# Kernel optimization log

Measured on AMD Instinct MI355X. Metric: run time of the kernel, lower is better.

The kernel has to match this reference:

```python
import jax, jax.numpy as jnp
import numpy as np
from jax import lax

SHIFT_SIZE = 5
PAD = SHIFT_SIZE // 2


def _shift(xn, axis):
    """xn: (B, C, Hp, Wp, Dp) zero-padded volume. Split channels into
    SHIFT_SIZE chunks and roll each chunk by shift in [-PAD, PAD] along `axis`."""
    chunks = jnp.split(xn, SHIFT_SIZE, axis=1)
    shifted = [jnp.roll(c, s, axis=axis) for c, s in zip(chunks, range(-PAD, PAD + 1))]
    return jnp.concatenate(shifted, axis=1)


def _shift_tokens(x, H, W, D, axis):
    """x: (B, N, C) tokens -> shifted tokens (B, N, C). axis=2 shifts H, axis=3 shifts W."""
    B, N, C = x.shape
    xn = x.transpose(0, 2, 1).reshape(B, C, H, W, D)
    xn = jnp.pad(xn, ((0, 0), (0, 0), (PAD, PAD), (PAD, PAD), (PAD, PAD)))
    xs = _shift(xn, axis)
    xs = xs[:, :, PAD:PAD + H, PAD:PAD + W, PAD:PAD + D]
    return xs.reshape(B, C, N).transpose(0, 2, 1)


def setup_inputs() -> dict:
    key = jax.random.key(0)
    ks = jax.random.split(key, 4)
    B, H, W, D = 2, 32, 32, 32
    N = H * W * D
    Cin, Ch = 160, 640
    return {
        "x": jax.random.normal(ks[0], (B, N, Cin), jnp.float32),
        "fc1_w": jax.random.normal(ks[1], (Ch, Cin), jnp.float32) * 0.02,
        "fc1_b": jnp.zeros((Ch,), jnp.float32),
        "dw_w": jax.random.normal(ks[2], (Ch, 1, 3, 3, 3), jnp.float32) * (2.0 / 27.0) ** 0.5,
        "dw_b": jnp.zeros((Ch,), jnp.float32),
        "fc2_w": jax.random.normal(ks[3], (Cin, Ch), jnp.float32) * 0.02,
        "fc2_b": jnp.zeros((Cin,), jnp.float32),
        "H": H, "W": W, "D": D,
    }


def reference(x, fc1_w, fc1_b, dw_w, dw_b, fc2_w, fc2_b, H, W, D):
    B, N, Cin = x.shape
    Ch = fc1_w.shape[0]
    # shift block 1: roll along H (axis 2)
    xs = _shift_tokens(x, H, W, D, axis=2)
    # fc1
    h = jnp.einsum('bnc,hc->bnh', xs, fc1_w) + fc1_b  # (B, N, Ch)
    # depthwise 3x3x3 conv
    hv = h.transpose(0, 2, 1).reshape(B, Ch, H, W, D)
    hv = lax.conv_general_dilated(
        hv, dw_w, window_strides=(1, 1, 1), padding='SAME',
        feature_group_count=Ch,
        dimension_numbers=('NCDHW', 'OIDHW', 'NCDHW'))
    hv = hv + dw_b[None, :, None, None, None]
    hv = jax.nn.gelu(hv, approximate=False)
    h = hv.reshape(B, Ch, N).transpose(0, 2, 1)
    # shift block 2: roll along W (axis 3)
    hs = _shift_tokens(h, H, W, D, axis=3)
    # fc2
    out = jnp.einsum('bnh,oh->bno', hs, fc2_w) + fc2_b  # (B, N, Cin)
    return out
```

## Files before the change

### kernel.cpp

```cpp
#include <hip/hip_runtime.h>
#include <hip/hip_bf16.h>
#include <math.h>

#define DEVI __device__ __forceinline__

typedef __bf16 bf16;
typedef _Float16 f16;
typedef bf16 bf16x4 __attribute__((ext_vector_type(4)));
typedef bf16 bf16x8 __attribute__((ext_vector_type(8)));
typedef f16 f16x8 __attribute__((ext_vector_type(8)));
typedef float f32x4 __attribute__((ext_vector_type(4)));

constexpr int Bb = 2, Hh = 32, Ww = 32, Dd = 32;
constexpr int Nn = Hh * Ww * Dd;
constexpr int BN = Bb * Nn;
constexpr int CIN = 160, CHH = 640;
constexpr int PD = 34;
constexpr int PT = PD * PD * PD;

constexpr size_t W1_OFF  = 0;
constexpr size_t W2_OFF  = W1_OFF + (size_t)CHH * CIN * 2;
constexpr size_t WTH_OFF = W2_OFF + (size_t)CIN * CHH * 2;
constexpr size_t ZP_OFF  = WTH_OFF + 34816;
constexpr size_t U_OFF   = 458752;
constexpr size_t H1P_OFF = U_OFF + (size_t)BN * CHH * 2;

DEVI void async16(const void* g, void* l) {
  __builtin_amdgcn_global_load_lds(
      (const __attribute__((address_space(1))) void*)g,
      (__attribute__((address_space(3))) void*)l, 16, 0, 0);
}

__global__ __launch_bounds__(256) void k_prep_x(const float* __restrict__ x,
                                                bf16* __restrict__ xb, int n4) {
  int i = blockIdx.x * 256 + threadIdx.x;
  if (i >= n4) return;
  float4 v = reinterpret_cast<const float4*>(x)[i];
  bf16x4 o;
  o[0] = (bf16)v.x; o[1] = (bf16)v.y; o[2] = (bf16)v.z; o[3] = (bf16)v.w;
  reinterpret_cast<bf16x4*>(xb)[i] = o;
}

__global__ __launch_bounds__(256) void k_prep_w(const float* __restrict__ fc1w,
                                                const float* __restrict__ fc2w,
                                                const float* __restrict__ dww,
                                                bf16* __restrict__ w1b,
                                                bf16* __restrict__ w2b,
                                                f16* __restrict__ wTh,
                                                unsigned* __restrict__ zp) {
  int i = blockIdx.x * 256 + threadIdx.x;
  const int NW = CHH * CIN;
  if (i < NW) {
    w1b[i] = (bf16)fc1w[i];
  } else if (i < 2 * NW) {
    int j = i - NW;
    w2b[j] = (bf16)fc2w[j];
  } else if (i < 2 * NW + 27 * CHH) {
    int j = i - 2 * NW;
    int ch = j / 27, tap = j % 27;
    wTh[tap * CHH + ch] = (f16)dww[j];
  } else if (i < 2 * NW + 27 * CHH + 2048) {
    zp[i - (2 * NW + 27 * CHH)] = 0u;
  }
}

__global__ __launch_bounds__(256) void k_zero_pad(f16* __restrict__ h1p) {
  int g = blockIdx.x * 256 + threadIdx.x;
  int p = g / 80;
  int c = g - p * 80;
  if (p >= 2 * PT) return;
  int r = p % PT;
  int hp = r / (PD * PD);
  int r2 = r % (PD * PD);
  int wp = r2 / PD, dp = r2 % PD;
  bool pad = (hp == 0) | (hp == PD - 1) | (wp == 0) | (wp == PD - 1) |
             (dp == 0) | (dp == PD - 1);
  if (!pad) return;
  f16x8 z = {};
  *(f16x8*)&h1p[(size_t)p * CHH + c * 8] = z;
}

__global__ __launch_bounds__(256) void k_gemm1(const bf16* __restrict__ xb,
                                               const bf16* __restrict__ w1b,
                                               const float* __restrict__ fc1b,
                                               const bf16* __restrict__ zp,
                                               f16* __restrict__ h1p) {
  __shared__ bf16 lsA[128 * 32];
  __shared__ bf16 lsB[128 * 32];
  const int tid = threadIdx.x;
  const int lane = tid & 63, wave = tid >> 6;
  const int row0 = blockIdx.x * 128;
  const int col0 = blockIdx.y * 128;

  f32x4 acc[4][4] = {};
  const int wr = wave >> 1, wc = wave & 1;
  const int rl = lane & 15, kb = (lane >> 4) * 8;

  for (int ks = 0; ks < 5; ++ks) {
    __syncthreads();
    const int s = ks - 2;
#pragma unroll
    for (int issue = 0; issue < 2; ++issue) {
      int c = issue * 256 + tid;
      int ar = c >> 2;
      int kc = (c & 3) * 8;
      int t = row0 + ar;
      int h = (t >> 10) & 31;
      int hs = h - s;
      const bf16* src;
      if (hs >= 0 && hs < 32)
        src = xb + (size_t)(t - s * 1024) * CIN + ks * 32 + kc;
      else
        src = zp + (size_t)(c & 63) * 8;
      async16(src, (char*)lsA + issue * 4096 + wave * 1024);
    }
#pragma unroll
    for (int issue = 0; issue < 2; ++issue) {
      int c = issue * 256 + tid;
      int br = c >> 2;
      int kc = (c & 3) * 8;
      const bf16* src = w1b + (size_t)(col0 + br) * CIN + ks * 32 + kc;
      async16(src, (char*)lsB + issue * 4096 + wave * 1024);
    }
    __syncthreads();
    bf16x8 af[4], bfr[4];
#pragma unroll
    for (int mi = 0; mi < 4; ++mi)
      af[mi] = *(const bf16x8*)&lsA[(wr * 64 + mi * 16 + rl) * 32 + kb];
#pragma unroll
    for (int ni = 0; ni < 4; ++ni)
      bfr[ni] = *(const bf16x8*)&lsB[(wc * 64 + ni * 16 + rl) * 32 + kb];
#pragma unroll
    for (int mi = 0; mi < 4; ++mi)
#pragma unroll
      for (int ni = 0; ni < 4; ++ni)
        acc[mi][ni] = __builtin_amdgcn_mfma_f32_16x16x32_bf16(af[mi], bfr[ni], acc[mi][ni], 0, 0, 0);
  }
  const int rq = lane >> 4;
#pragma unroll
  for (int mi = 0; mi < 4; ++mi) {
    int rowq = row0 + wr * 64 + mi * 16 + rq * 4;
    int bq = rowq >> 15;
    int nq = rowq & 32767;
    int hq = nq >> 10, wq = (nq >> 5) & 31, dq = nq & 31;
    size_t pos = (size_t)((bq * PD + hq + 1) * PD + (wq + 1)) * PD + (dq + 1);
    f16* dst0 = h1p + pos * CHH;
#pragma unroll
    for (int ni = 0; ni < 4; ++ni) {
      int col = col0 + wc * 64 + ni * 16 + rl;
      float bias = fc1b[col];
#pragma unroll
      for (int r = 0; r < 4; ++r)
        dst0[(size_t)r * CHH + col] = (f16)(acc[mi][ni][r] + bias);
    }
  }
}

__global__ __launch_bounds__(256) void k_conv(const f16* __restrict__ h1p,
                                              const f16* __restrict__ wTh,
                                              const float* __restrict__ dwb,
                                              bf16* __restrict__ h2b) {
  __shared__ f16 lw[27 * 64];
  __shared__ float lb[64];
  const int tid = threadIdx.x;
  const int cg = blockIdx.y;
#pragma unroll
  for (int i = 0; i < 7; ++i) {
    int idx = i * 256 + tid;
    if (idx < 27 * 64) lw[idx] = wTh[(idx >> 6) * CHH + cg * 64 + (idx & 63)];
  }
  if (tid < 64) lb[tid] = dwb[cg * 64 + tid];
  __syncthreads();

  const int lane = tid & 63, wave = tid >> 6;
  const int line = blockIdx.x * 4 + wave;
  const int c8 = lane & 7, dq = lane >> 3;
  const int d0 = dq * 4;
  const int ch0 = cg * 64 + c8 * 8;
  const int w = line & 31, h = (line >> 5) & 31, b = line >> 10;

  const size_t cidx = (size_t)((b * PD + h) * PD + w) * PD + d0;
  const f16* base = h1p + cidx * CHH + ch0;

  f16x8 acc[4];
  {
    f16x8 binit;
#pragma unroll
    for (int j = 0; j < 8; ++j) binit[j] = (f16)lb[c8 * 8 + j];
    acc[0] = binit; acc[1] = binit; acc[2] = binit; acc[3] = binit;
  }

#pragma unroll
  for (int kz = 0; kz < 3; ++kz) {
#pragma unroll
    for (int ky = 0; ky < 3; ++ky) {
      const f16* pb = base + (size_t)(kz * PD + ky) * PD * CHH;
      f16x8 wt[3];
#pragma unroll
      for (int kx = 0; kx < 3; ++kx)
        wt[kx] = *(const f16x8*)&lw[((kz * 9 + ky * 3 + kx) << 6) + c8 * 8];
      f16x8 v[6];
#pragma unroll
      for (int j = 0; j < 6; ++j)
        v[j] = *(const f16x8*)(pb + (size_t)j * CHH);
#pragma unroll
      for (int o = 0; o < 4; ++o)
#pragma unroll
        for (int kx = 0; kx < 3; ++kx)
          acc[o] = v[o + kx] * wt[kx] + acc[o];
    }
  }

  const ptrdiff_t obase = (ptrdiff_t)(line * 32 + d0) * CHH + ch0;
#pragma unroll
  for (int o = 0; o < 4; ++o) {
    bf16x8 ovec;
#pragma unroll
    for (int j = 0; j < 8; ++j) {
      float xv = (float)acc[o][j];
      float x2 = xv * xv;
      float u = xv * (2.3022078f + 0.102943324f * x2);
      float e = __builtin_exp2f(u);
      float r = __builtin_amdgcn_rcpf(1.0f + e);
      ovec[j] = (bf16)(xv - xv * r);
    }
    *(bf16x8*)&h2b[obase + (ptrdiff_t)o * CHH] = ovec;
  }
}

__global__ __launch_bounds__(256) void k_gemm2(const bf16* __restrict__ h2b,
                                               const bf16* __restrict__ w2b,
                                               const float* __restrict__ fc2b,
                                               const bf16* __restrict__ zp,
                                               float* __restrict__ out) {
  __shared__ bf16 lsA[128 * 64];
  __shared__ bf16 lsB[160 * 64];
  const int tid = threadIdx.x, lane = tid & 63, wave = tid >> 6;
  const int row0 = blockIdx.x * 128;
  const int rl = lane & 15, kb = (lane >> 4) * 8;

  f32x4 acc[2][10] = {};

  for (int kt = 0; kt < 10; ++kt) {
    __syncthreads();
    const int k0 = kt * 64;
    const int s = (k0 >> 7) - 2;
#pragma unroll
    for (int issue = 0; issue < 4; ++issue) {
      int c = issue * 256 + tid;
      int ar = c >> 3;
      int kc = (c & 7) * 8;
      int t = row0 + ar;
      int w = (t >> 5) & 31;
      int wsv = w - s;
      const bf16* src;
      if (wsv >= 0 && wsv < 32)
        src = h2b + (size_t)(t - s * 32) * CHH + k0 + kc;
      else
        src = zp + (size_t)(c & 63) * 8;
      async16(src, (char*)lsA + issue * 4096 + wave * 1024);
    }
#pragma unroll
    for (int issue = 0; issue < 5; ++issue) {
      int c = issue * 256 + tid;
      int br = c >> 3;
      int kc = (c & 7) * 8;
      const bf16* src = w2b + (size_t)br * CHH + k0 + kc;
      async16(src, (char*)lsB + issue * 4096 + wave * 1024);
    }
    __syncthreads();
#pragma unroll
    for (int kk = 0; kk < 2; ++kk) {
      bf16x8 af[2], bfr[10];
#pragma unroll
      for (int mi = 0; mi < 2; ++mi)
        af[mi] = *(const bf16x8*)&lsA[(wave * 32 + mi * 16 + rl) * 64 + kk * 32 + kb];
#pragma unroll
      for (int ni = 0; ni < 10; ++ni)
        bfr[ni] = *(const bf16x8*)&lsB[(ni * 16 + rl) * 64 + kk * 32 + kb];
#pragma unroll
      for (int mi = 0; mi < 2; ++mi)
#pragma unroll
        for (int ni = 0; ni < 10; ++ni)
          acc[mi][ni] = __builtin_amdgcn_mfma_f32_16x16x32_bf16(af[mi], bfr[ni], acc[mi][ni], 0, 0, 0);
    }
  }
  const int rq = lane >> 4;
#pragma unroll
  for (int mi = 0; mi < 2; ++mi) {
#pragma unroll
    for (int ni = 0; ni < 10; ++ni) {
      int col = ni * 16 + rl;
      float bias = fc2b[col];
#pragma unroll
      for (int r = 0; r < 4; ++r) {
        int row = row0 + wave * 32 + mi * 16 + rq * 4 + r;
        out[(size_t)row * CIN + col] = acc[mi][ni][r] + bias;
      }
    }
  }
}

extern "C" void kernel_launch(void* const* d_in, const int* in_sizes, int n_in,
                              void* d_out, int out_size, void* d_ws, size_t ws_size,
                              hipStream_t stream) {
  const float* x    = (const float*)d_in[0];
  const float* fc1w = (const float*)d_in[1];
  const float* fc1b = (const float*)d_in[2];
  const float* dww  = (const float*)d_in[3];
  const float* dwb  = (const float*)d_in[4];
  const float* fc2w = (const float*)d_in[5];
  const float* fc2b = (const float*)d_in[6];

  char* ws = (char*)d_ws;
  bf16* w1b  = (bf16*)(ws + W1_OFF);
  bf16* w2b  = (bf16*)(ws + W2_OFF);
  f16*  wTh  = (f16*)(ws + WTH_OFF);
  bf16* zp   = (bf16*)(ws + ZP_OFF);
  bf16* xb   = (bf16*)(ws + U_OFF);
  bf16* h2b  = (bf16*)(ws + U_OFF);
  f16*  h1p  = (f16*)(ws + H1P_OFF);
  float* out = (float*)d_out;

  k_zero_pad<<<(2 * PT * 80) / 256, 256, 0, stream>>>(h1p);
  k_prep_x<<<(BN * CIN / 4) / 256, 256, 0, stream>>>(x, xb, BN * CIN / 4);
  k_prep_w<<<943, 256, 0, stream>>>(fc1w, fc2w, dww, w1b, w2b, wTh, (unsigned*)zp);
  dim3 g1(512, 5);
  k_gemm1<<<g1, 256, 0, stream>>>(xb, w1b, fc1b, zp, h1p);
  dim3 gc(BN / 32 / 4, 10);
  k_conv<<<gc, 256, 0, stream>>>(h1p, wTh, dwb, h2b);
  k_gemm2<<<512, 256, 0, stream>>>(h2b, w2b, fc2b, zp, out);
}
```

Measured before the change: 146.0 us.

## Fuse x conversion into gemm1, switch GEMMs to fp16, prefetch conv rows

Removes the separate x-to-bf16 prep kernel. gemm1 now loads the fp32 input with the H-shift applied, converts it to fp16 into a full-K LDS tile, and loops over all five column tiles in one block, reusing the A tile. Both GEMMs change from bf16 to fp16 MFMA, and the conv intermediate becomes fp16. The depthwise conv software-prefetches the next row of inputs and packs its GELU output with cvt_pkrtz. The aim is to cut an extra pass over x and the five-fold A reloads, at the cost of larger LDS use, fewer gemm1 blocks and a risk of fp16 range limits.

```diff
diff --git a/kernel.cpp b/kernel.cpp
--- a/kernel.cpp
+++ b/kernel.cpp
@@ -4,10 +4,9 @@
 
 #define DEVI __device__ __forceinline__
 
-typedef __bf16 bf16;
 typedef _Float16 f16;
-typedef bf16 bf16x4 __attribute__((ext_vector_type(4)));
-typedef bf16 bf16x8 __attribute__((ext_vector_type(8)));
+typedef f16 f16x2 __attribute__((ext_vector_type(2)));
+typedef f16 f16x4 __attribute__((ext_vector_type(4)));
 typedef f16 f16x8 __attribute__((ext_vector_type(8)));
 typedef float f32x4 __attribute__((ext_vector_type(4)));
 
@@ -31,30 +30,20 @@
       (__attribute__((address_space(3))) void*)l, 16, 0, 0);
 }
 
-__global__ __launch_bounds__(256) void k_prep_x(const float* __restrict__ x,
-                                                bf16* __restrict__ xb, int n4) {
-  int i = blockIdx.x * 256 + threadIdx.x;
-  if (i >= n4) return;
-  float4 v = reinterpret_cast<const float4*>(x)[i];
-  bf16x4 o;
-  o[0] = (bf16)v.x; o[1] = (bf16)v.y; o[2] = (bf16)v.z; o[3] = (bf16)v.w;
-  reinterpret_cast<bf16x4*>(xb)[i] = o;
-}
-
 __global__ __launch_bounds__(256) void k_prep_w(const float* __restrict__ fc1w,
                                                 const float* __restrict__ fc2w,
                                                 const float* __restrict__ dww,
-                                                bf16* __restrict__ w1b,
-                                                bf16* __restrict__ w2b,
+                                                f16* __restrict__ w1h,
+                                                f16* __restrict__ w2h,
                                                 f16* __restrict__ wTh,
                                                 unsigned* __restrict__ zp) {
   int i = blockIdx.x * 256 + threadIdx.x;
   const int NW = CHH * CIN;
   if (i < NW) {
-    w1b[i] = (bf16)fc1w[i];
+    w1h[i] = (f16)fc1w[i];
   } else if (i < 2 * NW) {
     int j = i - NW;
-    w2b[j] = (bf16)fc2w[j];
+    w2h[j] = (f16)fc2w[j];
   } else if (i < 2 * NW + 27 * CHH) {
     int j = i - 2 * NW;
     int ch = j / 27, tap = j % 27;
@@ -80,78 +69,83 @@
   *(f16x8*)&h1p[(size_t)p * CHH + c * 8] = z;
 }
 
-__global__ __launch_bounds__(256) void k_gemm1(const bf16* __restrict__ xb,
-                                               const bf16* __restrict__ w1b,
+__global__ __launch_bounds__(256) void k_gemm1(const float* __restrict__ x,
+                                               const f16* __restrict__ w1h,
                                                const float* __restrict__ fc1b,
-                                               const bf16* __restrict__ zp,
                                                f16* __restrict__ h1p) {
-  __shared__ bf16 lsA[128 * 32];
-  __shared__ bf16 lsB[128 * 32];
+  constexpr int LDA = 168;
+  __shared__ f16 lsA[128 * LDA];
+  __shared__ f16 lsB[128 * 32];
   const int tid = threadIdx.x;
   const int lane = tid & 63, wave = tid >> 6;
   const int row0 = blockIdx.x * 128;
-  const int col0 = blockIdx.y * 128;
-
-  f32x4 acc[4][4] = {};
   const int wr = wave >> 1, wc = wave & 1;
   const int rl = lane & 15, kb = (lane >> 4) * 8;
 
-  for (int ks = 0; ks < 5; ++ks) {
-    __syncthreads();
-    const int s = ks - 2;
-#pragma unroll
-    for (int issue = 0; issue < 2; ++issue) {
-      int c = issue * 256 + tid;
-      int ar = c >> 2;
-      int kc = (c & 3) * 8;
-      int t = row0 + ar;
-      int h = (t >> 10) & 31;
-      int hs = h - s;
-      const bf16* src;
-      if (hs >= 0 && hs < 32)
-        src = xb + (size_t)(t - s * 1024) * CIN + ks * 32 + kc;
-      else
-        src = zp + (size_t)(c & 63) * 8;
-      async16(src, (char*)lsA + issue * 4096 + wave * 1024);
-    }
-#pragma unroll
-    for (int issue = 0; issue < 2; ++issue) {
-      int c = issue * 256 + tid;
-      int br = c >> 2;
-      int kc = (c & 3) * 8;
-      const bf16* src = w1b + (size_t)(col0 + br) * CIN + ks * 32 + kc;
-      async16(src, (char*)lsB + issue * 4096 + wave * 1024);
-    }
-    __syncthreads();
-    bf16x8 af[4], bfr[4];
-#pragma unroll
-    for (int mi = 0; mi < 4; ++mi)
-      af[mi] = *(const bf16x8*)&lsA[(wr * 64 + mi * 16 + rl) * 32 + kb];
-#pragma unroll
-    for (int ni = 0; ni < 4; ++ni)
-      bfr[ni] = *(const bf16x8*)&lsB[(wc * 64 + ni * 16 + rl) * 32 + kb];
-#pragma unroll
-    for (int mi = 0; mi < 4; ++mi)
+#pragma unroll
+  for (int i = 0; i < 20; ++i) {
+    int c = i * 256 + tid;
+    int row = c / 40;
+    int q = c - row * 40;
+    int ch0 = q * 4;
+    int ks = ch0 >> 5;
+    int s = ks - 2;
+    int t = row0 + row;
+    int h = (t >> 10) & 31;
+    int hs = h - s;
+    float4 v = {0.f, 0.f, 0.f, 0.f};
+    if (hs >= 0 && hs < 32)
+      v = *(const float4*)&x[(long)(t - s * 1024) * CIN + ch0];
+    f16x4 o4;
+    o4[0] = (f16)v.x; o4[1] = (f16)v.y; o4[2] = (f16)v.z; o4[3] = (f16)v.w;
+    *(f16x4*)&lsA[row * LDA + ch0] = o4;
+  }
+  __syncthreads();
+
+  for (int nt = 0; nt < 5; ++nt) {
+    const int col0 = nt * 128;
+    f32x4 acc[4][4] = {};
+    for (int ks = 0; ks < 5; ++ks) {
+#pragma unroll
+      for (int issue = 0; issue < 2; ++issue) {
+        int c = issue * 256 + tid;
+        int br = c >> 2;
+        int kc = (c & 3) * 8;
+        const f16* src = w1h + (size_t)(col0 + br) * CIN + ks * 32 + kc;
+        async16(src, (char*)lsB + issue * 4096 + wave * 1024);
+      }
+      __syncthreads();
+      f16x8 af[4], bfr[4];
+#pragma unroll
+      for (int mi = 0; mi < 4; ++mi)
+        af[mi] = *(const f16x8*)&lsA[(wr * 64 + mi * 16 + rl) * LDA + ks * 32 + kb];
 #pragma unroll
       for (int ni = 0; ni < 4; ++ni)
-        acc[mi][ni] = __builtin_amdgcn_mfma_f32_16x16x32_bf16(af[mi], bfr[ni], acc[mi][ni], 0, 0, 0);
-  }
-  const int rq = lane >> 4;
-#pragma unroll
-  for (int mi = 0; mi < 4; ++mi) {
-    int rowq = row0 + wr * 64 + mi * 16 + rq * 4;
-    int bq = rowq >> 15;
-    int nq = rowq & 32767;
-    int hq = nq >> 10, wq = (nq >> 5) & 31, dq = nq & 31;
-    size_t pos = (size_t)((bq * PD + hq + 1) * PD + (wq + 1)) * PD + (dq + 1);
-    f16* dst0 = h1p + pos * CHH;
-#pragma unroll
-    for (int ni = 0; ni < 4; ++ni) {
-      int col = col0 + wc * 64 + ni * 16 + rl;
-      float bias = fc1b[col];
-#pragma unroll
-      for (int r = 0; r < 4; ++r)
-        dst0[(size_t)r * CHH + col] = (f16)(acc[mi][ni][r] + bias);
+        bfr[ni] = *(const f16x8*)&lsB[(wc * 64 + ni * 16 + rl) * 32 + kb];
+#pragma unroll
+      for (int mi = 0; mi < 4; ++mi)
+#pragma unroll
+        for (int ni = 0; ni < 4; ++ni)
+          acc[mi][ni] = __builtin_amdgcn_mfma_f32_16x16x32_f16(af[mi], bfr[ni], acc[mi][ni], 0, 0, 0);
+      __syncthreads();
+    }
+    const int rq = lane >> 4;
+#pragma unroll
+    for (int mi = 0; mi < 4; ++mi) {
+      int rowq = row0 + wr * 64 + mi * 16 + rq * 4;
+      int bq = rowq >> 15;
+      int nq = rowq & 32767;
+      int hq = nq >> 10, wq = (nq >> 5) & 31, dq = nq & 31;
+      size_t pos = (size_t)((bq * PD + hq + 1) * PD + (wq + 1)) * PD + (dq + 1);
+      f16* dst0 = h1p + pos * CHH;
+#pragma unroll
+      for (int ni = 0; ni < 4; ++ni) {
+        int col = col0 + wc * 64 + ni * 16 + rl;
+        float bias = fc1b[col];
+#pragma unroll
+        for (int r = 0; r < 4; ++r)
+          dst0[(size_t)r * CHH + col] = (f16)(acc[mi][ni][r] + bias);
+      }
     }
   }
 }
@@ -159,9 +153,9 @@
 __global__ __launch_bounds__(256) void k_conv(const f16* __restrict__ h1p,
                                               const f16* __restrict__ wTh,
                                               const float* __restrict__ dwb,
-                                              bf16* __restrict__ h2b) {
+                                              f16* __restrict__ h2h) {
   __shared__ f16 lw[27 * 64];
-  __shared__ float lb[64];
+  __shared__ f16 lb[64];
   const int tid = threadIdx.x;
   const int cg = blockIdx.y;
 #pragma unroll
@@ -169,7 +163,7 @@
     int idx = i * 256 + tid;
     if (idx < 27 * 64) lw[idx] = wTh[(idx >> 6) * CHH + cg * 64 + (idx & 63)];
   }
-  if (tid < 64) lb[tid] = dwb[cg * 64 + tid];
+  if (tid < 64) lb[tid] = (f16)dwb[cg * 64 + tid];
   __syncthreads();
 
   const int lane = tid & 63, wave = tid >> 6;
@@ -184,57 +178,69 @@
 
   f16x8 acc[4];
   {
-    f16x8 binit;
-#pragma unroll
-    for (int j = 0; j < 8; ++j) binit[j] = (f16)lb[c8 * 8 + j];
+    f16x8 binit = *(const f16x8*)&lb[c8 * 8];
     acc[0] = binit; acc[1] = binit; acc[2] = binit; acc[3] = binit;
   }
 
-#pragma unroll
-  for (int kz = 0; kz < 3; ++kz) {
-#pragma unroll
-    for (int ky = 0; ky < 3; ++ky) {
-      const f16* pb = base + (size_t)(kz * PD + ky) * PD * CHH;
-      f16x8 wt[3];
-#pragma unroll
-      for (int kx = 0; kx < 3; ++kx)
-        wt[kx] = *(const f16x8*)&lw[((kz * 9 + ky * 3 + kx) << 6) + c8 * 8];
-      f16x8 v[6];
+  f16x8 v[6], vn[6];
+#pragma unroll
+  for (int j = 0; j < 6; ++j)
+    v[j] = *(const f16x8*)(base + (size_t)j * CHH);
+
+#pragma unroll
+  for (int p = 0; p < 9; ++p) {
+    const int kz = p / 3, ky = p % 3;
+    if (p < 8) {
+      const int kz2 = (p + 1) / 3, ky2 = (p + 1) % 3;
+      const f16* pb2 = base + (size_t)(kz2 * PD + ky2) * PD * CHH;
 #pragma unroll
       for (int j = 0; j < 6; ++j)
-        v[j] = *(const f16x8*)(pb + (size_t)j * CHH);
-#pragma unroll
-      for (int o = 0; o < 4; ++o)
-#pragma unroll
-        for (int kx = 0; kx < 3; ++kx)
-          acc[o] = v[o + kx] * wt[kx] + acc[o];
-    }
+        vn[j] = *(const f16x8*)(pb2 + (size_t)j * CHH);
+    }
+    f16x8 wt0 = *(const f16x8*)&lw[((kz * 9 + ky * 3 + 0) << 6) + c8 * 8];
+    f16x8 wt1 = *(const f16x8*)&lw[((kz * 9 + ky * 3 + 1) << 6) + c8 * 8];
+    f16x8 wt2 = *(const f16x8*)&lw[((kz * 9 + ky * 3 + 2) << 6) + c8 * 8];
+#pragma unroll
+    for (int o = 0; o < 4; ++o) {
+      acc[o] = v[o] * wt0 + acc[o];
+      acc[o] = v[o + 1] * wt1 + acc[o];
+      acc[o] = v[o + 2] * wt2 + acc[o];
+    }
+#pragma unroll
+    for (int j = 0; j < 6; ++j) v[j] = vn[j];
   }
 
   const ptrdiff_t obase = (ptrdiff_t)(line * 32 + d0) * CHH + ch0;
 #pragma unroll
   for (int o = 0; o < 4; ++o) {
-    bf16x8 ovec;
-#pragma unroll
-    for (int j = 0; j < 8; ++j) {
-      float xv = (float)acc[o][j];
-      float x2 = xv * xv;
-      float u = xv * (2.3022078f + 0.102943324f * x2);
-      float e = __builtin_exp2f(u);
-      float r = __builtin_amdgcn_rcpf(1.0f + e);
-      ovec[j] = (bf16)(xv - xv * r);
-    }
-    *(bf16x8*)&h2b[obase + (ptrdiff_t)o * CHH] = ovec;
-  }
-}
-
-__global__ __launch_bounds__(256) void k_gemm2(const bf16* __restrict__ h2b,
-                                               const bf16* __restrict__ w2b,
+    f16x8 xa = acc[o];
+    f16x8 ov;
+#pragma unroll
+    for (int j = 0; j < 8; j += 2) {
+      float g01[2];
+#pragma unroll
+      for (int u2 = 0; u2 < 2; ++u2) {
+        float xv = (float)xa[j + u2];
+        float x2 = xv * xv;
+        float uu = xv * (2.3022078f + 0.102943324f * x2);
+        float e = __builtin_exp2f(uu);
+        float r = __builtin_amdgcn_rcpf(1.0f + e);
+        g01[u2] = xv - xv * r;
+      }
+      f16x2 pk = __builtin_bit_cast(f16x2, __builtin_amdgcn_cvt_pkrtz(g01[0], g01[1]));
+      ov[j] = pk[0]; ov[j + 1] = pk[1];
+    }
+    *(f16x8*)&h2h[obase + (ptrdiff_t)o * CHH] = ov;
+  }
+}
+
+__global__ __launch_bounds__(256) void k_gemm2(const f16* __restrict__ h2h,
+                                               const f16* __restrict__ w2h,
                                                const float* __restrict__ fc2b,
-                                               const bf16* __restrict__ zp,
+                                               const f16* __restrict__ zp,
                                                float* __restrict__ out) {
-  __shared__ bf16 lsA[128 * 64];
-  __shared__ bf16 lsB[160 * 64];
+  __shared__ f16 lsA[128 * 64];
+  __shared__ f16 lsB[160 * 64];
   const int tid = threadIdx.x, lane = tid & 63, wave = tid >> 6;
   const int row0 = blockIdx.x * 128;
   const int rl = lane & 15, kb = (lane >> 4) * 8;
@@ -253,9 +259,9 @@
       int t = row0 + ar;
       int w = (t >> 5) & 31;
       int wsv = w - s;
-      const bf16* src;
+      const f16* src;
       if (wsv >= 0 && wsv < 32)
-        src = h2b + (size_t)(t - s * 32) * CHH + k0 + kc;
+        src = h2h + (size_t)(t - s * 32) * CHH + k0 + kc;
       else
         src = zp + (size_t)(c & 63) * 8;
       async16(src, (char*)lsA + issue * 4096 + wave * 1024);
@@ -265,24 +271,24 @@
       int c = issue * 256 + tid;
       int br = c >> 3;
       int kc = (c & 7) * 8;
-      const bf16* src = w2b + (size_t)br * CHH + k0 + kc;
+      const f16* src = w2h + (size_t)br * CHH + k0 + kc;
       async16(src, (char*)lsB + issue * 4096 + wave * 1024);
     }
     __syncthreads();
 #pragma unroll
     for (int kk = 0; kk < 2; ++kk) {
-      bf16x8 af[2], bfr[10];
+      f16x8 af[2], bfr[10];
 #pragma unroll
       for (int mi = 0; mi < 2; ++mi)
-        af[mi] = *(const bf16x8*)&lsA[(wave * 32 + mi * 16 + rl) * 64 + kk * 32 + kb];
+        af[mi] = *(const f16x8*)&lsA[(wave * 32 + mi * 16 + rl) * 64 + kk * 32 + kb];
 #pragma unroll
       for (int ni = 0; ni < 10; ++ni)
-        bfr[ni] = *(const bf16x8*)&lsB[(ni * 16 + rl) * 64 + kk * 32 + kb];
+        bfr[ni] = *(const f16x8*)&lsB[(ni * 16 + rl) * 64 + kk * 32 + kb];
 #pragma unroll
       for (int mi = 0; mi < 2; ++mi)
 #pragma unroll
         for (int ni = 0; ni < 10; ++ni)
-          acc[mi][ni] = __builtin_amdgcn_mfma_f32_16x16x32_bf16(af[mi], bfr[ni], acc[mi][ni], 0, 0, 0);
+          acc[mi][ni] = __builtin_amdgcn_mfma_f32_16x16x32_f16(af[mi], bfr[ni], acc[mi][ni], 0, 0, 0);
     }
   }
   const int rq = lane >> 4;
@@ -313,21 +319,18 @@
   const float* fc2b = (const float*)d_in[6];
 
   char* ws = (char*)d_ws;
-  bf16* w1b  = (bf16*)(ws + W1_OFF);
-  bf16* w2b  = (bf16*)(ws + W2_OFF);
-  f16*  wTh  = (f16*)(ws + WTH_OFF);
-  bf16* zp   = (bf16*)(ws + ZP_OFF);
-  bf16* xb   = (bf16*)(ws + U_OFF);
-  bf16* h2b  = (bf16*)(ws + U_OFF);
-  f16*  h1p  = (f16*)(ws + H1P_OFF);
+  f16* w1h  = (f16*)(ws + W1_OFF);
+  f16* w2h  = (f16*)(ws + W2_OFF);
+  f16* wTh  = (f16*)(ws + WTH_OFF);
+  f16* zp   = (f16*)(ws + ZP_OFF);
+  f16* h2h  = (f16*)(ws + U_OFF);
+  f16* h1p  = (f16*)(ws + H1P_OFF);
   float* out = (float*)d_out;
 
   k_zero_pad<<<(2 * PT * 80) / 256, 256, 0, stream>>>(h1p);
-  k_prep_x<<<(BN * CIN / 4) / 256, 256, 0, stream>>>(x, xb, BN * CIN / 4);
-  k_prep_w<<<943, 256, 0, stream>>>(fc1w, fc2w, dww, w1b, w2b, wTh, (unsigned*)zp);
-  dim3 g1(512, 5);
-  k_gemm1<<<g1, 256, 0, stream>>>(xb, w1b, fc1b, zp, h1p);
+  k_prep_w<<<876, 256, 0, stream>>>(fc1w, fc2w, dww, w1h, w2h, wTh, (unsigned*)zp);
+  k_gemm1<<<512, 256, 0, stream>>>(x, w1h, fc1b, h1p);
   dim3 gc(BN / 32 / 4, 10);
-  k_conv<<<gc, 256, 0, stream>>>(h1p, wTh, dwb, h2b);
-  k_gemm2<<<512, 256, 0, stream>>>(h2b, w2b, fc2b, zp, out);
-}
+  k_conv<<<gc, 256, 0, stream>>>(h1p, wTh, dwb, h2h);
+  k_gemm2<<<512, 256, 0, stream>>>(h2h, w2h, fc2b, zp, out);
+}
```

After: 156.8 us. +7.4%, slower.
